# Performance work log

Measured on AMD Instinct MI355X. Metric: run time of the kernel, lower is better.

Reference implementation:

```python
import jax, jax.numpy as jnp
import numpy as np

B, CDD, HIS, T, L, D, K = 64, 5, 100, 30, 3, 256, 10
THRESHOLD = 0.1


def setup_inputs() -> dict:
    key = jax.random.key(0)
    k1, k2, k3, k4 = jax.random.split(key, 4)
    cdd_repr = jax.random.normal(k1, (B, CDD, D), dtype=jnp.float32)
    his_repr = jax.random.normal(k2, (B, HIS, D), dtype=jnp.float32)
    his_embedding = jax.random.normal(k3, (B, HIS, T, L, D), dtype=jnp.float32)
    # xavier_normal init for Linear(D, D)
    W_sel = jax.random.normal(k4, (D, D), dtype=jnp.float32) * np.sqrt(2.0 / (D + D))
    b_sel = jnp.zeros((D,), dtype=jnp.float32)
    return {"cdd_repr": cdd_repr, "his_repr": his_repr,
            "his_embedding": his_embedding, "W_sel": W_sel, "b_sel": b_sel}


def _l2_normalize(x, eps=1e-12):
    # matches torch F.normalize(dim=-1)
    n = jnp.linalg.norm(x, axis=-1, keepdims=True)
    return x / jnp.maximum(n, eps)


def reference(cdd_repr, his_repr, his_embedding, W_sel, b_sel):
    # selectionProject (Linear) + L2 normalize
    cdd_p = _l2_normalize(cdd_repr @ W_sel.T + b_sel)   # [B, CDD, D]
    his_p = _l2_normalize(his_repr @ W_sel.T + b_sel)   # [B, HIS, D]

    # news-level attention scores [B, CDD, HIS]
    attn = jnp.einsum('bcd,bhd->bch', cdd_p, his_p)

    # top-k over history
    attn_topk, idx = jax.lax.top_k(attn, K)             # [B, CDD, K]

    # multi-dim gather of history embeddings -> [B, CDD, K, T, L, D]
    his_activated = his_embedding[jnp.arange(B)[:, None, None], idx]

    # threshold masking: zero out weights below threshold, scale embeddings
    w = jnp.where(attn_topk < THRESHOLD, 0.0, attn_topk)
    his_activated = his_activated * w[:, :, :, None, None, None]

    return his_activated, idx
```

## Files before the change

kernel.cpp:

```cpp
#include <hip/hip_runtime.h>
#include <hip/hip_bf16.h>

#define NB   64
#define NCDD 5
#define NHIS 100
#define ND   256
#define NK   10
#define TLD  23040
#define THRESH 0.1f
#define NEG_INF (-3.402823466e38f)
#define NROWS_HIS 6400
#define NROWS_CDD 320

typedef float f32x4 __attribute__((ext_vector_type(4)));

__global__ __launch_bounds__(256) void proj_norm_all(
    const float* __restrict__ his_repr,
    const float* __restrict__ cdd_repr,
    const float* __restrict__ W,
    const float* __restrict__ bvec,
    float* __restrict__ Yall)
{
    __shared__ float red[4][8];
    const int r0  = blockIdx.x * 8;
    const int tid = threadIdx.x;

    const float* __restrict__ X = (r0 < NROWS_HIS)
        ? (his_repr + (size_t)r0 * ND)
        : (cdd_repr + (size_t)(r0 - NROWS_HIS) * ND);

    const float bias = bvec[tid];
    float acc[8];
#pragma unroll
    for (int r = 0; r < 8; ++r) acc[r] = bias;

    const float* wrow = W + (size_t)tid * ND;
    for (int k = 0; k < ND; k += 4) {
        const float4 w4 = *(const float4*)(wrow + k);
#pragma unroll
        for (int r = 0; r < 8; ++r) {
            const float4 x4 = *(const float4*)(X + (size_t)r * ND + k);
            acc[r] += w4.x * x4.x + w4.y * x4.y + w4.z * x4.z + w4.w * x4.w;
        }
    }

    const int wave = tid >> 6, lane = tid & 63;
#pragma unroll
    for (int r = 0; r < 8; ++r) {
        float v = acc[r] * acc[r];
        for (int off = 32; off; off >>= 1) v += __shfl_xor(v, off);
        if (lane == 0) red[wave][r] = v;
    }
    __syncthreads();

#pragma unroll
    for (int r = 0; r < 8; ++r) {
        const float s = red[0][r] + red[1][r] + red[2][r] + red[3][r];
        const float scale = 1.0f / fmaxf(sqrtf(s), 1e-12f);
        Yall[(size_t)(r0 + r) * ND + tid] = acc[r] * scale;
    }
}

__global__ __launch_bounds__(512) void attn_topk_kernel(
    const float* __restrict__ cdd_p,
    const float* __restrict__ his_p,
    float* __restrict__ out_idx_f,
    int* __restrict__ ws_idx,
    float* __restrict__ ws_w)
{
    __shared__ f32x4 cdds[NCDD * 64];
    __shared__ float attn_s[NCDD][128];
    const int b   = blockIdx.x;
    const int tid = threadIdx.x;

    for (int i = tid; i < NCDD * 64; i += 512)
        cdds[i] = ((const f32x4*)(cdd_p + (size_t)b * NCDD * ND))[i];
    __syncthreads();

    if (tid < NCDD * NHIS) {
        const int c = tid / NHIS, h = tid % NHIS;
        const f32x4* __restrict__ hrow =
            (const f32x4*)(his_p + ((size_t)b * NHIS + h) * ND);
        float a0 = 0.f, a1 = 0.f, a2 = 0.f, a3 = 0.f;
#pragma unroll 8
        for (int k = 0; k < 64; k += 4) {
            const f32x4 c0 = cdds[c * 64 + k],     h0 = hrow[k];
            const f32x4 c1 = cdds[c * 64 + k + 1], h1 = hrow[k + 1];
            const f32x4 c2 = cdds[c * 64 + k + 2], h2 = hrow[k + 2];
            const f32x4 c3 = cdds[c * 64 + k + 3], h3 = hrow[k + 3];
            a0 += c0[0]*h0[0] + c0[1]*h0[1] + c0[2]*h0[2] + c0[3]*h0[3];
            a1 += c1[0]*h1[0] + c1[1]*h1[1] + c1[2]*h1[2] + c1[3]*h1[3];
            a2 += c2[0]*h2[0] + c2[1]*h2[1] + c2[2]*h2[2] + c2[3]*h2[3];
            a3 += c3[0]*h3[0] + c3[1]*h3[1] + c3[2]*h3[2] + c3[3]*h3[3];
        }
        attn_s[c][h] = (a0 + a1) + (a2 + a3);
    }
    __syncthreads();

    const int wave = tid >> 6, lane = tid & 63;
    if (wave < NCDD) {
        const int c = wave;
        float v0 = attn_s[c][lane];
        float v1 = (lane + 64 < NHIS) ? attn_s[c][lane + 64] : NEG_INF;
#pragma unroll
        for (int k = 0; k < NK; ++k) {
            float lv; int li;
            if (v1 > v0) { lv = v1; li = lane + 64; }
            else         { lv = v0; li = lane; }
            for (int off = 1; off < 64; off <<= 1) {
                const float ov = __shfl_xor(lv, off);
                const int   oi = __shfl_xor(li, off);
                if (ov > lv || (ov == lv && oi < li)) { lv = ov; li = oi; }
            }
            if (lane == 0) {
                const float w = (lv < THRESH) ? 0.0f : lv;
                const int g = (b * NCDD + c) * NK + k;
                ws_idx[g] = li;
                ws_w[g]   = w;
                out_idx_f[g] = (float)li;
            }
            if (li == lane)            v0 = NEG_INF;
            else if (li == lane + 64)  v1 = NEG_INF;
        }
    }
}

__global__ __launch_bounds__(256) void gather_kernel(
    const float* __restrict__ his_emb,
    const int* __restrict__ ws_idx,
    const float* __restrict__ ws_w,
    float* __restrict__ out)
{
    const int orig = blockIdx.x;
    const int g = (orig & 7) * 400 + (orig >> 3);
    const int b = g / (NCDD * NK);
    const int tid = threadIdx.x;
    const float w = ws_w[g];

    f32x4* __restrict__ dst = (f32x4*)(out + (size_t)g * TLD);

    if (w == 0.0f) {
        const f32x4 z = {0.f, 0.f, 0.f, 0.f};
#pragma unroll
        for (int it = 0; it < 22; ++it) dst[tid + it * 256] = z;
        if (tid < 128) dst[22 * 256 + tid] = z;
        return;
    }

    const int idx = ws_idx[g];
    const f32x4* __restrict__ src =
        (const f32x4*)(his_emb + ((size_t)b * NHIS + idx) * TLD);

    f32x4 v[8];
#pragma unroll
    for (int j = 0; j < 8; ++j) v[j] = src[tid + j * 256];
#pragma unroll
    for (int j = 0; j < 8; ++j) dst[tid + j * 256] = v[j] * w;
#pragma unroll
    for (int j = 0; j < 8; ++j) v[j] = src[tid + (8 + j) * 256];
#pragma unroll
    for (int j = 0; j < 8; ++j) dst[tid + (8 + j) * 256] = v[j] * w;
#pragma unroll
    for (int j = 0; j < 6; ++j) v[j] = src[tid + (16 + j) * 256];
#pragma unroll
    for (int j = 0; j < 6; ++j) dst[tid + (16 + j) * 256] = v[j] * w;
    if (tid < 128) {
        const int i = 22 * 256 + tid;
        f32x4 t = src[i];
        dst[i] = t * w;
    }
}

extern "C" void kernel_launch(void* const* d_in, const int* in_sizes, int n_in,
                              void* d_out, int out_size, void* d_ws, size_t ws_size,
                              hipStream_t stream)
{
    const float* cdd_repr = (const float*)d_in[0];
    const float* his_repr = (const float*)d_in[1];
    const float* his_emb  = (const float*)d_in[2];
    const float* W_sel    = (const float*)d_in[3];
    const float* b_sel    = (const float*)d_in[4];
    float* out = (float*)d_out;

    char* ws = (char*)d_ws;
    float* Yall  = (float*)ws;
    float* his_p = Yall;
    float* cdd_p = Yall + (size_t)NROWS_HIS * ND;
    int*   idx_i = (int*)  (ws + 6881280);
    float* w_w   = (float*)(ws + 6894080);

    float* out_idx_f = out + (size_t)NB * NCDD * NK * TLD;

    proj_norm_all<<<(NROWS_HIS + NROWS_CDD) / 8, 256, 0, stream>>>(
        his_repr, cdd_repr, W_sel, b_sel, Yall);
    attn_topk_kernel<<<NB, 512, 0, stream>>>(cdd_p, his_p,
                                             out_idx_f, idx_i, w_w);
    gather_kernel<<<NB * NCDD * NK, 256, 0, stream>>>(his_emb, idx_i, w_w, out);
}
```

Measured before the change: 173.3 us.

## Split projection and attention dot products across 4-lane groups for coalesced loads

The projection kernel now has each group of 4 lanes split the K dimension of one output row, and each thread computes 4 output columns instead of 1. Partial sums are combined with lane shuffles, which makes the W and X loads contiguous across neighbouring lanes instead of strided per thread. The attention kernel likewise assigns 4 lanes to each (cdd, his) dot product, reads cdd rows straight from global memory instead of staging them in shared memory, and reduces with shuffles. This costs extra shuffles and redundant row-norm work (sums are scaled by 0.25 to undo the 4x duplication). Only the small front kernels change; the gather kernel, which moves most of the bytes, is untouched.

```diff
diff --git a/kernel.cpp b/kernel.cpp
--- a/kernel.cpp
+++ b/kernel.cpp
@@ -24,40 +24,80 @@
     __shared__ float red[4][8];
     const int r0  = blockIdx.x * 8;
     const int tid = threadIdx.x;
+    const int sub = tid & 3;
+    const int grp = tid >> 2;
+    const int wave = tid >> 6, lane = tid & 63;
 
     const float* __restrict__ X = (r0 < NROWS_HIS)
         ? (his_repr + (size_t)r0 * ND)
         : (cdd_repr + (size_t)(r0 - NROWS_HIS) * ND);
 
-    const float bias = bvec[tid];
-    float acc[8];
-#pragma unroll
-    for (int r = 0; r < 8; ++r) acc[r] = bias;
-
-    const float* wrow = W + (size_t)tid * ND;
-    for (int k = 0; k < ND; k += 4) {
-        const float4 w4 = *(const float4*)(wrow + k);
+    float acc[4][8];
+#pragma unroll
+    for (int p = 0; p < 4; ++p)
+#pragma unroll
+        for (int r = 0; r < 8; ++r) acc[p][r] = 0.f;
+
+#pragma unroll 4
+    for (int i = 0; i < 16; ++i) {
+        const int kb = sub * 4 + 16 * i;
+        float4 x4[8];
+#pragma unroll
+        for (int r = 0; r < 8; ++r)
+            x4[r] = *(const float4*)(X + (size_t)r * ND + kb);
+#pragma unroll
+        for (int p = 0; p < 4; ++p) {
+            const int d = p * 64 + grp;
+            const float4 w4 = *(const float4*)(W + (size_t)d * ND + kb);
+#pragma unroll
+            for (int r = 0; r < 8; ++r)
+                acc[p][r] += w4.x * x4[r].x + w4.y * x4[r].y
+                           + w4.z * x4[r].z + w4.w * x4[r].w;
+        }
+    }
+
+#pragma unroll
+    for (int p = 0; p < 4; ++p)
 #pragma unroll
         for (int r = 0; r < 8; ++r) {
-            const float4 x4 = *(const float4*)(X + (size_t)r * ND + k);
-            acc[r] += w4.x * x4.x + w4.y * x4.y + w4.z * x4.z + w4.w * x4.w;
-        }
-    }
-
-    const int wave = tid >> 6, lane = tid & 63;
+            float v = acc[p][r];
+            v += __shfl_xor(v, 1);
+            v += __shfl_xor(v, 2);
+            acc[p][r] = v;
+        }
+
+    float bias[4];
+#pragma unroll
+    for (int p = 0; p < 4; ++p) bias[p] = bvec[p * 64 + grp];
+
+    float ss[8];
 #pragma unroll
     for (int r = 0; r < 8; ++r) {
-        float v = acc[r] * acc[r];
-        for (int off = 32; off; off >>= 1) v += __shfl_xor(v, off);
-        if (lane == 0) red[wave][r] = v;
+        float t = 0.f;
+#pragma unroll
+        for (int p = 0; p < 4; ++p) {
+            const float y = acc[p][r] + bias[p];
+            acc[p][r] = y;
+            t += y * y;
+        }
+        for (int off = 32; off; off >>= 1) t += __shfl_xor(t, off);
+        ss[r] = t;
+    }
+    if (lane == 0) {
+#pragma unroll
+        for (int r = 0; r < 8; ++r) red[wave][r] = ss[r];
     }
     __syncthreads();
 
 #pragma unroll
     for (int r = 0; r < 8; ++r) {
-        const float s = red[0][r] + red[1][r] + red[2][r] + red[3][r];
+        const float s = 0.25f * (red[0][r] + red[1][r] + red[2][r] + red[3][r]);
         const float scale = 1.0f / fmaxf(sqrtf(s), 1e-12f);
-        Yall[(size_t)(r0 + r) * ND + tid] = acc[r] * scale;
+        if (sub == 0) {
+#pragma unroll
+            for (int p = 0; p < 4; ++p)
+                Yall[(size_t)(r0 + r) * ND + p * 64 + grp] = acc[p][r] * scale;
+        }
     }
 }
 
@@ -68,36 +108,37 @@
     int* __restrict__ ws_idx,
     float* __restrict__ ws_w)
 {
-    __shared__ f32x4 cdds[NCDD * 64];
     __shared__ float attn_s[NCDD][128];
     const int b   = blockIdx.x;
     const int tid = threadIdx.x;
-
-    for (int i = tid; i < NCDD * 64; i += 512)
-        cdds[i] = ((const f32x4*)(cdd_p + (size_t)b * NCDD * ND))[i];
+    const int sub = tid & 3, grp = tid >> 2;
+    const int wave = tid >> 6, lane = tid & 63;
+
+    const float* __restrict__ cbase = cdd_p + (size_t)b * NCDD * ND;
+    const float* __restrict__ hbase = his_p + (size_t)b * NHIS * ND;
+
+#pragma unroll
+    for (int it = 0; it < 4; ++it) {
+        const int task = it * 128 + grp;
+        if (task < NCDD * NHIS) {
+            const int c = task / NHIS, h = task - c * NHIS;
+            const float* __restrict__ crow = cbase + (size_t)c * ND;
+            const float* __restrict__ hrow = hbase + (size_t)h * ND;
+            float a = 0.f;
+#pragma unroll
+            for (int i = 0; i < 16; ++i) {
+                const int kb = sub * 4 + 16 * i;
+                const float4 cv = *(const float4*)(crow + kb);
+                const float4 hv = *(const float4*)(hrow + kb);
+                a += cv.x * hv.x + cv.y * hv.y + cv.z * hv.z + cv.w * hv.w;
+            }
+            a += __shfl_xor(a, 1);
+            a += __shfl_xor(a, 2);
+            if (sub == 0) attn_s[c][h] = a;
+        }
+    }
     __syncthreads();
 
-    if (tid < NCDD * NHIS) {
-        const int c = tid / NHIS, h = tid % NHIS;
-        const f32x4* __restrict__ hrow =
-            (const f32x4*)(his_p + ((size_t)b * NHIS + h) * ND);
-        float a0 = 0.f, a1 = 0.f, a2 = 0.f, a3 = 0.f;
-#pragma unroll 8
-        for (int k = 0; k < 64; k += 4) {
-            const f32x4 c0 = cdds[c * 64 + k],     h0 = hrow[k];
-            const f32x4 c1 = cdds[c * 64 + k + 1], h1 = hrow[k + 1];
-            const f32x4 c2 = cdds[c * 64 + k + 2], h2 = hrow[k + 2];
-            const f32x4 c3 = cdds[c * 64 + k + 3], h3 = hrow[k + 3];
-            a0 += c0[0]*h0[0] + c0[1]*h0[1] + c0[2]*h0[2] + c0[3]*h0[3];
-            a1 += c1[0]*h1[0] + c1[1]*h1[1] + c1[2]*h1[2] + c1[3]*h1[3];
-            a2 += c2[0]*h2[0] + c2[1]*h2[1] + c2[2]*h2[2] + c2[3]*h2[3];
-            a3 += c3[0]*h3[0] + c3[1]*h3[1] + c3[2]*h3[2] + c3[3]*h3[3];
-        }
-        attn_s[c][h] = (a0 + a1) + (a2 + a3);
-    }
-    __syncthreads();
-
-    const int wave = tid >> 6, lane = tid & 63;
     if (wave < NCDD) {
         const int c = wave;
         float v0 = attn_s[c][lane];
```

Result: faster. 165.6 us (-4.4%).
